# Kernel tuning notes

Measured on AMD Instinct MI355X. Metric: run time of the kernel, lower is better.

## Reference

```python
import jax, jax.numpy as jnp
import numpy as np

N_NODES = 100000
N_EDGES = 400000
IN_FEATS = 64
H_FEATS = 128
INTER = 128
NUM_CLASSES = 64


def setup_inputs() -> dict:
    key = jax.random.key(0)
    ks = jax.random.split(key, 32)
    inp = {}
    inp['gate_type'] = jax.random.randint(ks[0], (N_NODES,), 0, IN_FEATS)
    inp['src'] = jax.random.randint(ks[1], (N_EDGES,), 0, N_NODES)
    inp['dst'] = jax.random.randint(ks[2], (N_EDGES,), 0, N_NODES)
    inp['src_idx'] = jax.random.uniform(ks[3], (N_EDGES,), dtype=jnp.float32)
    inp['dst_idx'] = jax.random.uniform(ks[4], (N_EDGES,), dtype=jnp.float32)
    inp['rev'] = jax.random.uniform(ks[5], (N_EDGES,), dtype=jnp.float32)
    inp['emb'] = jax.random.normal(ks[6], (IN_FEATS, IN_FEATS), dtype=jnp.float32) * 0.05
    dims = [(IN_FEATS, H_FEATS), (H_FEATS, H_FEATS), (H_FEATS, H_FEATS), (H_FEATS, H_FEATS), (H_FEATS, NUM_CLASSES)]
    k = 7
    for i, (fi, fo) in enumerate(dims, 1):
        # xavier-normal-like scaling
        inp[f'w1_{i}'] = jax.random.normal(ks[k], (INTER, fi + 3), dtype=jnp.float32) * np.float32(np.sqrt(2.0 / (fi + 3 + INTER))); k += 1
        inp[f'w2_{i}'] = jax.random.normal(ks[k], (fo, fi + INTER), dtype=jnp.float32) * np.float32(np.sqrt(2.0 / (fi + INTER + fo))); k += 1
        inp[f'b2_{i}'] = jnp.zeros((fo,), dtype=jnp.float32); k += 1
    return inp


def _qconv(h, src, dst, w_edge, W1, W2, b2):
    # message: concat src node feats with edge feats -> [E, d+3]
    m = jnp.concatenate([h[src], w_edge], axis=1)
    # linear1 (no bias) + leaky_relu (torch default slope 0.01)
    tmp = jax.nn.leaky_relu(m @ W1.T, negative_slope=0.01)  # [E, inter]
    # mean-reduce per destination node (isolated nodes -> zeros, matching DGL)
    s = jax.ops.segment_sum(tmp, dst, num_segments=h.shape[0])
    cnt = jax.ops.segment_sum(jnp.ones((dst.shape[0],), tmp.dtype), dst, num_segments=h.shape[0])
    h_N = s / jnp.maximum(cnt, 1.0)[:, None]
    # linear2 on [h, h_N]
    return jnp.concatenate([h, h_N], axis=1) @ W2.T + b2


def reference(gate_type, src, dst, src_idx, dst_idx, rev, emb,
              w1_1, w2_1, b2_1, w1_2, w2_2, b2_2, w1_3, w2_3, b2_3,
              w1_4, w2_4, b2_4, w1_5, w2_5, b2_5):
    h = emb[gate_type]  # [N, in_feats]
    w_edge = jnp.stack([src_idx, dst_idx, rev], axis=1)  # [E, 3]
    layers = [(w1_1, w2_1, b2_1), (w1_2, w2_2, b2_2), (w1_3, w2_3, b2_3),
              (w1_4, w2_4, b2_4), (w1_5, w2_5, b2_5)]
    for i, (W1, W2, b2) in enumerate(layers):
        h = _qconv(h, src, dst, w_edge, W1, W2, b2)
        if i < 4:
            h = jax.nn.relu(h)
    return h
```

## Files before the change

kernel.cpp:

```cpp
#include <hip/hip_runtime.h>
#include <hip/hip_fp16.h>

typedef __attribute__((ext_vector_type(8))) short short8;
typedef __attribute__((ext_vector_type(4))) float f32x4;
typedef unsigned short u16;

__device__ __forceinline__ u16 f2bf(float f) {
    unsigned u = __float_as_uint(f);
    unsigned r = ((u >> 16) & 1) + 0x7FFFu;
    return (u16)((u + r) >> 16);
}

__device__ __forceinline__ void gload_lds16(const void* g, void* l) {
    __builtin_amdgcn_global_load_lds((const __attribute__((address_space(1))) unsigned int*)g,
                                     (__attribute__((address_space(3))) unsigned int*)l,
                                     16, 0, 0);
}

__device__ __forceinline__ unsigned pk_fma(unsigned a, unsigned b, unsigned c) {
    unsigned d;
    asm("v_pk_fma_f16 %0, %1, %2, %3" : "=v"(d) : "v"(a), "v"(b), "v"(c));
    return d;
}
__device__ __forceinline__ unsigned pk_mul(unsigned a, unsigned b) {
    unsigned d;
    asm("v_pk_mul_f16 %0, %1, %2" : "=v"(d) : "v"(a), "v"(b));
    return d;
}
__device__ __forceinline__ unsigned pk_max(unsigned a, unsigned b) {
    unsigned d;
    asm("v_pk_max_f16 %0, %1, %2" : "=v"(d) : "v"(a), "v"(b));
    return d;
}


__global__ void k_count(const int* __restrict__ dst, int* __restrict__ cnt, int E) {
    int i = blockIdx.x * 256 + threadIdx.x;
    if (i < E) atomicAdd(&cnt[dst[i]], 1);
}

__global__ void k_scan1(const int* __restrict__ cnt, int* __restrict__ partial, int N) {
    __shared__ int sm[256];
    int idx = blockIdx.x * 256 + threadIdx.x;
    sm[threadIdx.x] = (idx < N) ? cnt[idx] : 0;
    __syncthreads();
    for (int s = 128; s > 0; s >>= 1) {
        if (threadIdx.x < s) sm[threadIdx.x] += sm[threadIdx.x + s];
        __syncthreads();
    }
    if (threadIdx.x == 0) partial[blockIdx.x] = sm[0];
}

__global__ void k_scan2(int* __restrict__ partial, int nb) {
    __shared__ int sm[512];
    int t = threadIdx.x;
    sm[t] = (t < nb) ? partial[t] : 0;
    __syncthreads();
    for (int off = 1; off < 512; off <<= 1) {
        int v = (t >= off) ? sm[t - off] : 0;
        __syncthreads();
        sm[t] += v;
        __syncthreads();
    }
    if (t < nb) partial[t] = (t == 0) ? 0 : sm[t - 1];
}

__global__ void k_scan3(const int* __restrict__ cnt, const int* __restrict__ partial,
                        int* __restrict__ row_off, int* __restrict__ cursor,
                        float* __restrict__ invdeg, int N, int E) {
    __shared__ int sm[256];
    int idx = blockIdx.x * 256 + threadIdx.x;
    int v = (idx < N) ? cnt[idx] : 0;
    sm[threadIdx.x] = v;
    __syncthreads();
    for (int off = 1; off < 256; off <<= 1) {
        int u = (threadIdx.x >= off) ? sm[threadIdx.x - off] : 0;
        __syncthreads();
        sm[threadIdx.x] += u;
        __syncthreads();
    }
    if (idx < N) {
        int excl = partial[blockIdx.x] + sm[threadIdx.x] - v;
        row_off[idx] = excl;
        cursor[idx] = excl;
        invdeg[idx] = 1.0f / (float)((v > 1) ? v : 1);
    }
    if (idx == 0) row_off[N] = E;
}

__global__ void k_scatter(const int* __restrict__ dst, const int* __restrict__ src,
                          const float* __restrict__ sidx, const float* __restrict__ didx,
                          const float* __restrict__ rev,
                          int* __restrict__ cursor, int4* __restrict__ payload, int E) {
    int i = blockIdx.x * 256 + threadIdx.x;
    if (i < E) {
        int p = atomicAdd(&cursor[dst[i]], 1);
        unsigned hs = (unsigned)__half_as_ushort(__float2half_rn(sidx[i]));
        unsigned hd = (unsigned)__half_as_ushort(__float2half_rn(didx[i]));
        unsigned hr = (unsigned)__half_as_ushort(__float2half_rn(rev[i]));
        int4 v;
        v.x = src[i];
        v.y = (int)(hs * 0x10001u);
        v.z = (int)(hd * 0x10001u);
        v.w = (int)(hr * 0x10001u);
        payload[p] = v;
    }
}


__global__ void k_emb(const int* __restrict__ gt, const float* __restrict__ emb,
                      u16* __restrict__ h0, int N) {
    int i = blockIdx.x * 256 + threadIdx.x;
    if (i < N * 64) {
        int n = i >> 6, f = i & 63;
        h0[i] = f2bf(emb[(gt[n] << 6) | f]);
    }
}


struct WDesc {
    const float* src[10];
    u16* dst[10];
    int scols[10];
    int dcols[10];
    int n[10];
};

__global__ void k_wconv(WDesc d) {
    int seg = blockIdx.y;
    int idx = blockIdx.x * 256 + threadIdx.x;
    if (idx < d.n[seg]) {
        int dc = d.dcols[seg];
        int r = idx / dc, c = idx % dc;
        d.dst[seg][idx] = f2bf(d.src[seg][r * d.scols[seg] + c]);
    }
}

struct EDesc {
    const float* src[5];
    unsigned* dst[5];
    int ldw[5];
    int fi[5];
};

__global__ void k_wedge(EDesc d) {
    int l = blockIdx.x;
    int i = threadIdx.x;
    if (i < 192) {
        int c = i >> 6, j = i & 63;
        float a = d.src[l][(size_t)(2 * j) * d.ldw[l] + d.fi[l] + c];
        float b = d.src[l][(size_t)(2 * j + 1) * d.ldw[l] + d.fi[l] + c];
        unsigned lo = (unsigned)__half_as_ushort(__float2half_rn(a));
        unsigned hi = (unsigned)__half_as_ushort(__float2half_rn(b));
        d.dst[l][(c << 6) + j] = lo | (hi << 16);
    }
}


__global__ __launch_bounds__(256)
void k_edge(int N,
            const int* __restrict__ row_off, const int4* __restrict__ payload,
            const u16* __restrict__ g,
            const unsigned* __restrict__ W1h,
            const float* __restrict__ invdeg,
            u16* __restrict__ hN)
{
    const int t = threadIdx.x;
    const int lane = t & 63;
    const int fl = lane & 15;
    const int eg = lane >> 4;
    const int wid = blockIdx.x * (blockDim.x >> 6) + (t >> 6);
    const int nwtot = gridDim.x * (blockDim.x >> 6);
    const int per = (N + nwtot - 1) / nwtot;
    const int n0 = wid * per;
    if (n0 >= N) return;
    const int n1 = (n0 + per < N) ? (n0 + per) : N;

    const uint4 wa = *(const uint4*)&W1h[(fl << 2)];
    const uint4 wb = *(const uint4*)&W1h[64 + (fl << 2)];
    const uint4 wc = *(const uint4*)&W1h[128 + (fl << 2)];
    const unsigned c001 = ((unsigned)__half_as_ushort(__float2half_rn(0.01f))) * 0x10001u;

    int beg = row_off[n0];
    for (int n = n0; n < n1; ++n) {
        const int end = row_off[n + 1];
        float acc[8] = {0.f, 0.f, 0.f, 0.f, 0.f, 0.f, 0.f, 0.f};

        int p = beg + eg;
        int4 pl;
        if (p < end) pl = payload[p];
        while (p < end) {
            const int pn = p + 4;
            int4 plN = pl;
            if (pn < end) plN = payload[pn];
            const uint4 gv = *(const uint4*)(g + ((size_t)pl.x << 7) + (fl << 3));
            const unsigned si = (unsigned)pl.y;
            const unsigned di = (unsigned)pl.z;
            const unsigned rv = (unsigned)pl.w;
            unsigned v0 = pk_fma(wa.x, si, gv.x);
            unsigned v1 = pk_fma(wa.y, si, gv.y);
            unsigned v2 = pk_fma(wa.z, si, gv.z);
            unsigned v3 = pk_fma(wa.w, si, gv.w);
            v0 = pk_fma(wb.x, di, v0);
            v1 = pk_fma(wb.y, di, v1);
            v2 = pk_fma(wb.z, di, v2);
            v3 = pk_fma(wb.w, di, v3);
            v0 = pk_fma(wc.x, rv, v0);
            v1 = pk_fma(wc.y, rv, v1);
            v2 = pk_fma(wc.z, rv, v2);
            v3 = pk_fma(wc.w, rv, v3);
            v0 = pk_max(v0, pk_mul(v0, c001));
            v1 = pk_max(v1, pk_mul(v1, c001));
            v2 = pk_max(v2, pk_mul(v2, c001));
            v3 = pk_max(v3, pk_mul(v3, c001));
            const float2 f0 = __half22float2(*(const __half2*)&v0);
            const float2 f1 = __half22float2(*(const __half2*)&v1);
            const float2 f2 = __half22float2(*(const __half2*)&v2);
            const float2 f3 = __half22float2(*(const __half2*)&v3);
            acc[0] += f0.x; acc[1] += f0.y;
            acc[2] += f1.x; acc[3] += f1.y;
            acc[4] += f2.x; acc[5] += f2.y;
            acc[6] += f3.x; acc[7] += f3.y;
            p = pn;
            pl = plN;
        }

#pragma unroll
        for (int r = 0; r < 8; r++) {
            acc[r] += __shfl_xor(acc[r], 16, 64);
            acc[r] += __shfl_xor(acc[r], 32, 64);
        }

        if (eg == 0) {
            const float inv = invdeg[n];
            unsigned q0 = (unsigned)f2bf(acc[0] * inv) | ((unsigned)f2bf(acc[1] * inv) << 16);
            unsigned q1 = (unsigned)f2bf(acc[2] * inv) | ((unsigned)f2bf(acc[3] * inv) << 16);
            unsigned q2 = (unsigned)f2bf(acc[4] * inv) | ((unsigned)f2bf(acc[5] * inv) << 16);
            unsigned q3 = (unsigned)f2bf(acc[6] * inv) | ((unsigned)f2bf(acc[7] * inv) << 16);
            uint4 out = make_uint4(q0, q1, q2, q3);
            *(uint4*)(hN + ((size_t)n << 7) + (fl << 3)) = out;
        }
        beg = end;
    }
}


template<int K, int O, int SPLIT, int BIAS, int RELU, int OUTDT>
__global__ __launch_bounds__(256)
void k_mfma(int M,
            const u16* __restrict__ A1, int lda1,
            const u16* __restrict__ A2, int lda2,
            const u16* __restrict__ Wb,
            const float* __restrict__ bias,
            void* __restrict__ Cout, int ldc)
{
    constexpr int KP = K + 8;
    constexpr int NF = O / 32;
    constexpr int WC = O / 2;
    __shared__ __align__(16) u16 Wlds[O * KP];
    __shared__ __align__(16) u16 Atile[128 * 32];

    const int t = threadIdx.x;
    const int m0 = blockIdx.x * 128;
    const int w = t >> 6, l = t & 63;
    const int wm = w & 1, wn = w >> 1;
    const int lr = l & 15, lh = l >> 4;

    for (int idx = t; idx < O * (K / 8); idx += 256) {
        int row = idx / (K / 8), ch = idx % (K / 8);
        uint4 v = *(const uint4*)(Wb + (size_t)row * K + ch * 8);
        *(uint4*)(&Wlds[row * KP + ch * 8]) = v;
    }

    f32x4 acc[4][NF];
#pragma unroll
    for (int mi = 0; mi < 4; mi++)
#pragma unroll
        for (int ni = 0; ni < NF; ni++) acc[mi][ni] = (f32x4){0.f, 0.f, 0.f, 0.f};

    __syncthreads();

    for (int kt = 0; kt < K / 32; ++kt) {
        const int k0 = kt * 32;
        const u16* Asrc;
        int lda, kof;
        if (k0 < SPLIT) { Asrc = A1; lda = lda1; kof = k0; }
        else            { Asrc = A2; lda = lda2; kof = k0 - SPLIT; }
#pragma unroll
        for (int q = 0; q < 2; ++q) {
            int o = q * 4096 + t * 16;
            int row = o >> 6, cb = o & 63;
            int m = m0 + row;
            m = (m < M) ? m : (M - 1);
            gload_lds16(Asrc + (size_t)m * lda + kof + (cb >> 1), (void*)(Atile + (o >> 1)));
        }
        __syncthreads();

        short8 a[4], b[NF];
#pragma unroll
        for (int mi = 0; mi < 4; mi++)
            a[mi] = *(const short8*)(Atile + (wm * 64 + mi * 16 + lr) * 32 + lh * 8);
#pragma unroll
        for (int ni = 0; ni < NF; ni++)
            b[ni] = *(const short8*)(Wlds + (size_t)(wn * WC + ni * 16 + lr) * KP + k0 + lh * 8);
#pragma unroll
        for (int mi = 0; mi < 4; mi++)
#pragma unroll
            for (int ni = 0; ni < NF; ni++)
                acc[mi][ni] = __builtin_amdgcn_mfma_f32_16x16x32_bf16(a[mi], b[ni], acc[mi][ni], 0, 0, 0);
        __syncthreads();
    }

    float bv[NF];
#pragma unroll
    for (int ni = 0; ni < NF; ni++)
        bv[ni] = BIAS ? bias[wn * WC + ni * 16 + lr] : 0.f;
#pragma unroll
    for (int mi = 0; mi < 4; mi++) {
#pragma unroll
        for (int i = 0; i < 4; i++) {
            int row = m0 + wm * 64 + mi * 16 + lh * 4 + i;
            if (row < M) {
#pragma unroll
                for (int ni = 0; ni < NF; ni++) {
                    float v = acc[mi][ni][i] + bv[ni];
                    if (RELU) v = fmaxf(v, 0.f);
                    int col = wn * WC + ni * 16 + lr;
                    if (OUTDT == 1)      ((u16*)Cout)[(size_t)row * ldc + col] = f2bf(v);
                    else if (OUTDT == 2) ((__half*)Cout)[(size_t)row * ldc + col] = __float2half(v);
                    else                 ((float*)Cout)[(size_t)row * ldc + col] = v;
                }
            }
        }
    }
}


extern "C" void kernel_launch(void* const* d_in, const int* in_sizes, int n_in,
                              void* d_out, int out_size, void* d_ws, size_t ws_size,
                              hipStream_t stream)
{
    const int N = in_sizes[0];
    const int E = in_sizes[1];
    const int* gate = (const int*)d_in[0];
    const int* src = (const int*)d_in[1];
    const int* dst = (const int*)d_in[2];
    const float* sidx = (const float*)d_in[3];
    const float* didx = (const float*)d_in[4];
    const float* rev = (const float*)d_in[5];
    const float* emb = (const float*)d_in[6];
    const float* w1[5] = {(const float*)d_in[7], (const float*)d_in[10], (const float*)d_in[13],
                          (const float*)d_in[16], (const float*)d_in[19]};
    const float* w2[5] = {(const float*)d_in[8], (const float*)d_in[11], (const float*)d_in[14],
                          (const float*)d_in[17], (const float*)d_in[20]};
    const float* b2[5] = {(const float*)d_in[9], (const float*)d_in[12], (const float*)d_in[15],
                          (const float*)d_in[18], (const float*)d_in[21]};

    char* ws = (char*)d_ws;
    size_t off = 0;
    auto alloc = [&](size_t bytes) {
        void* p = ws + off;
        off = (off + bytes + 255) & ~(size_t)255;
        return p;
    };
    u16* hb0 = (u16*)alloc((size_t)N * 128 * 2);
    u16* hb1 = (u16*)alloc((size_t)N * 128 * 2);
    u16* hN = (u16*)alloc((size_t)N * 128 * 2);
    u16* g = (u16*)alloc((size_t)N * 128 * 2);
    int* cnt = (int*)alloc((size_t)N * 4);
    int* row_off = (int*)alloc((size_t)(N + 1) * 4);
    int* cursor = (int*)alloc((size_t)N * 4);
    int4* payload = (int4*)alloc((size_t)E * 16);
    int* partial = (int*)alloc(512 * 4);
    float* invd = (float*)alloc((size_t)N * 4);
    unsigned* w1h = (unsigned*)alloc(5 * 192 * 4);
    u16* w1b[5];
    u16* w2b[5];
    const int fis[5] = {64, 128, 128, 128, 128};
    for (int i = 0; i < 5; i++) w1b[i] = (u16*)alloc((size_t)128 * fis[i] * 2);
    for (int i = 0; i < 5; i++) {
        int fo = (i == 4) ? 64 : 128;
        w2b[i] = (u16*)alloc((size_t)fo * (fis[i] + 128) * 2);
    }

    WDesc wd;
    for (int i = 0; i < 5; i++) {
        wd.src[i] = w1[i]; wd.dst[i] = w1b[i];
        wd.scols[i] = fis[i] + 3; wd.dcols[i] = fis[i]; wd.n[i] = 128 * fis[i];
        int fo = (i == 4) ? 64 : 128;
        wd.src[5 + i] = w2[i]; wd.dst[5 + i] = w2b[i];
        wd.scols[5 + i] = fis[i] + 128; wd.dcols[5 + i] = fis[i] + 128;
        wd.n[5 + i] = fo * (fis[i] + 128);
    }
    k_wconv<<<dim3(128, 10), dim3(256), 0, stream>>>(wd);

    EDesc ed;
    for (int i = 0; i < 5; i++) {
        ed.src[i] = w1[i];
        ed.dst[i] = w1h + i * 192;
        ed.ldw[i] = fis[i] + 3;
        ed.fi[i] = fis[i];
    }
    k_wedge<<<dim3(5), dim3(192), 0, stream>>>(ed);

    hipMemsetAsync(cnt, 0, (size_t)N * 4, stream);
    k_count<<<dim3((E + 255) / 256), dim3(256), 0, stream>>>(dst, cnt, E);
    const int nb = (N + 255) / 256;
    k_scan1<<<dim3(nb), dim3(256), 0, stream>>>(cnt, partial, N);
    k_scan2<<<dim3(1), dim3(512), 0, stream>>>(partial, nb);
    k_scan3<<<dim3(nb), dim3(256), 0, stream>>>(cnt, partial, row_off, cursor, invd, N, E);
    k_scatter<<<dim3((E + 255) / 256), dim3(256), 0, stream>>>(dst, src, sidx, didx, rev, cursor, payload, E);
    k_emb<<<dim3((N * 64 + 255) / 256), dim3(256), 0, stream>>>(gate, emb, hb0, N);

    u16* hcur = hb0;
    u16* hnxt = hb1;
    const int gg = (N + 127) / 128;
    const int eb = 2048;

    k_mfma<64, 128, 64, 0, 0, 2><<<dim3(gg), dim3(256), 0, stream>>>(
        N, hcur, 64, (const u16*)nullptr, 0, w1b[0], (const float*)nullptr, g, 128);
    k_edge<<<dim3(eb), dim3(256), 0, stream>>>(N, row_off, payload, g, w1h + 0 * 192, invd, hN);
    k_mfma<192, 128, 64, 1, 1, 1><<<dim3(gg), dim3(256), 0, stream>>>(
        N, hcur, 64, hN, 128, w2b[0], b2[0], hnxt, 128);
    hcur = hb1; hnxt = hb0;

    for (int l = 1; l < 4; ++l) {
        k_mfma<128, 128, 128, 0, 0, 2><<<dim3(gg), dim3(256), 0, stream>>>(
            N, hcur, 128, (const u16*)nullptr, 0, w1b[l], (const float*)nullptr, g, 128);
        k_edge<<<dim3(eb), dim3(256), 0, stream>>>(N, row_off, payload, g, w1h + l * 192, invd, hN);
        k_mfma<256, 128, 128, 1, 1, 1><<<dim3(gg), dim3(256), 0, stream>>>(
            N, hcur, 128, hN, 128, w2b[l], b2[l], hnxt, 128);
        u16* tmp = hcur; hcur = hnxt; hnxt = tmp;
    }

    k_mfma<128, 128, 128, 0, 0, 2><<<dim3(gg), dim3(256), 0, stream>>>(
        N, hcur, 128, (const u16*)nullptr, 0, w1b[4], (const float*)nullptr, g, 128);
    k_edge<<<dim3(eb), dim3(256), 0, stream>>>(N, row_off, payload, g, w1h + 4 * 192, invd, hN);
    k_mfma<256, 64, 128, 1, 0, 0><<<dim3(gg), dim3(256), 0, stream>>>(
        N, hcur, 128, hN, 128, w2b[4], b2[4], (float*)d_out, 64);
}
```

Measured before the change: 454.8 us.

## Fuse layer output GEMM with next layer's node projection GEMM

Adds a fused kernel that computes the linear2 output for a 128-row tile, applies bias and ReLU, writes h, and keeps the tile in LDS. It then multiplies that tile by the next layer's W1 node weights to produce the fp16 per-node projection used by the edge kernel. This removes four separate projection GEMM launches and the re-read of h from global memory. In exchange the kernel uses more LDS, aliasing the W tile with the H tile, which may lower occupancy and serialises two GEMMs within each block.

```diff
diff --git a/kernel.cpp b/kernel.cpp
--- a/kernel.cpp
+++ b/kernel.cpp
@@ -336,6 +336,143 @@
 }
 
 
+template<int K, int SPLIT>
+__global__ __launch_bounds__(256)
+void k_mfma_fused(int M,
+                  const u16* __restrict__ A1, int lda1,
+                  const u16* __restrict__ A2, int lda2,
+                  const u16* __restrict__ Wb,
+                  const float* __restrict__ bias,
+                  u16* __restrict__ Hout,
+                  const u16* __restrict__ Wg,
+                  u16* __restrict__ Gout)
+{
+    constexpr int KP = K + 8;
+    constexpr int HP = 136;
+    __shared__ __align__(16) char U[(128 * HP * 2) * 2 + 128 * 32 * 2];
+    u16* Wlds  = (u16*)U;
+    u16* Htile = (u16*)U;
+    u16* Wglds = (u16*)(U + 128 * HP * 2);
+    u16* Atile = (u16*)(U + 2 * 128 * HP * 2);
+
+    const int t = threadIdx.x;
+    const int m0 = blockIdx.x * 128;
+    const int w = t >> 6, l = t & 63;
+    const int wm = w & 1, wn = w >> 1;
+    const int lr = l & 15, lh = l >> 4;
+
+    for (int idx = t; idx < 128 * (K / 8); idx += 256) {
+        int row = idx / (K / 8), ch = idx % (K / 8);
+        uint4 v = *(const uint4*)(Wb + (size_t)row * K + ch * 8);
+        *(uint4*)(&Wlds[row * KP + ch * 8]) = v;
+    }
+
+    f32x4 acc[4][4];
+#pragma unroll
+    for (int mi = 0; mi < 4; mi++)
+#pragma unroll
+        for (int ni = 0; ni < 4; ni++) acc[mi][ni] = (f32x4){0.f, 0.f, 0.f, 0.f};
+
+    __syncthreads();
+
+    for (int kt = 0; kt < K / 32; ++kt) {
+        const int k0 = kt * 32;
+        const u16* Asrc;
+        int lda, kof;
+        if (k0 < SPLIT) { Asrc = A1; lda = lda1; kof = k0; }
+        else            { Asrc = A2; lda = lda2; kof = k0 - SPLIT; }
+#pragma unroll
+        for (int q = 0; q < 2; ++q) {
+            int o = q * 4096 + t * 16;
+            int row = o >> 6, cb = o & 63;
+            int m = m0 + row;
+            m = (m < M) ? m : (M - 1);
+            gload_lds16(Asrc + (size_t)m * lda + kof + (cb >> 1), (void*)(Atile + (o >> 1)));
+        }
+        __syncthreads();
+
+        short8 a[4], b[4];
+#pragma unroll
+        for (int mi = 0; mi < 4; mi++)
+            a[mi] = *(const short8*)(Atile + (wm * 64 + mi * 16 + lr) * 32 + lh * 8);
+#pragma unroll
+        for (int ni = 0; ni < 4; ni++)
+            b[ni] = *(const short8*)(Wlds + (size_t)(wn * 64 + ni * 16 + lr) * KP + k0 + lh * 8);
+#pragma unroll
+        for (int mi = 0; mi < 4; mi++)
+#pragma unroll
+            for (int ni = 0; ni < 4; ni++)
+                acc[mi][ni] = __builtin_amdgcn_mfma_f32_16x16x32_bf16(a[mi], b[ni], acc[mi][ni], 0, 0, 0);
+        __syncthreads();
+    }
+
+    for (int idx = t; idx < 128 * 16; idx += 256) {
+        int row = idx >> 4, ch = idx & 15;
+        uint4 v = *(const uint4*)(Wg + (size_t)row * 128 + ch * 8);
+        *(uint4*)(&Wglds[row * HP + ch * 8]) = v;
+    }
+
+    float bv[4];
+#pragma unroll
+    for (int ni = 0; ni < 4; ni++) bv[ni] = bias[wn * 64 + ni * 16 + lr];
+#pragma unroll
+    for (int mi = 0; mi < 4; mi++) {
+#pragma unroll
+        for (int i = 0; i < 4; i++) {
+            int rloc = wm * 64 + mi * 16 + lh * 4 + i;
+            int row = m0 + rloc;
+#pragma unroll
+            for (int ni = 0; ni < 4; ni++) {
+                float v = fmaxf(acc[mi][ni][i] + bv[ni], 0.f);
+                u16 hv = f2bf(v);
+                int col = wn * 64 + ni * 16 + lr;
+                Htile[rloc * HP + col] = hv;
+                if (row < M) Hout[(size_t)row * 128 + col] = hv;
+            }
+        }
+    }
+    __syncthreads();
+
+    f32x4 acc2[4][4];
+#pragma unroll
+    for (int mi = 0; mi < 4; mi++)
+#pragma unroll
+        for (int ni = 0; ni < 4; ni++) acc2[mi][ni] = (f32x4){0.f, 0.f, 0.f, 0.f};
+
+#pragma unroll
+    for (int kt = 0; kt < 4; ++kt) {
+        const int k0 = kt * 32;
+        short8 a[4], b[4];
+#pragma unroll
+        for (int mi = 0; mi < 4; mi++)
+            a[mi] = *(const short8*)(Htile + (wm * 64 + mi * 16 + lr) * HP + k0 + lh * 8);
+#pragma unroll
+        for (int ni = 0; ni < 4; ni++)
+            b[ni] = *(const short8*)(Wglds + (wn * 64 + ni * 16 + lr) * HP + k0 + lh * 8);
+#pragma unroll
+        for (int mi = 0; mi < 4; mi++)
+#pragma unroll
+            for (int ni = 0; ni < 4; ni++)
+                acc2[mi][ni] = __builtin_amdgcn_mfma_f32_16x16x32_bf16(a[mi], b[ni], acc2[mi][ni], 0, 0, 0);
+    }
+
+#pragma unroll
+    for (int mi = 0; mi < 4; mi++) {
+#pragma unroll
+        for (int i = 0; i < 4; i++) {
+            int row = m0 + wm * 64 + mi * 16 + lh * 4 + i;
+            if (row < M) {
+#pragma unroll
+                for (int ni = 0; ni < 4; ni++) {
+                    int col = wn * 64 + ni * 16 + lr;
+                    ((__half*)Gout)[(size_t)row * 128 + col] = __float2half(acc2[mi][ni][i]);
+                }
+            }
+        }
+    }
+}
+
+
 extern "C" void kernel_launch(void* const* d_in, const int* in_sizes, int n_in,
                               void* d_out, int out_size, void* d_ws, size_t ws_size,
                               hipStream_t stream)
@@ -412,29 +549,24 @@
     k_scatter<<<dim3((E + 255) / 256), dim3(256), 0, stream>>>(dst, src, sidx, didx, rev, cursor, payload, E);
     k_emb<<<dim3((N * 64 + 255) / 256), dim3(256), 0, stream>>>(gate, emb, hb0, N);
 
-    u16* hcur = hb0;
-    u16* hnxt = hb1;
     const int gg = (N + 127) / 128;
     const int eb = 2048;
 
     k_mfma<64, 128, 64, 0, 0, 2><<<dim3(gg), dim3(256), 0, stream>>>(
-        N, hcur, 64, (const u16*)nullptr, 0, w1b[0], (const float*)nullptr, g, 128);
+        N, hb0, 64, (const u16*)nullptr, 0, w1b[0], (const float*)nullptr, g, 128);
     k_edge<<<dim3(eb), dim3(256), 0, stream>>>(N, row_off, payload, g, w1h + 0 * 192, invd, hN);
-    k_mfma<192, 128, 64, 1, 1, 1><<<dim3(gg), dim3(256), 0, stream>>>(
-        N, hcur, 64, hN, 128, w2b[0], b2[0], hnxt, 128);
-    hcur = hb1; hnxt = hb0;
-
+    k_mfma_fused<192, 64><<<dim3(gg), dim3(256), 0, stream>>>(
+        N, hb0, 64, hN, 128, w2b[0], b2[0], hb1, w1b[1], g);
+
+    u16* hcur = hb1;
+    u16* hnxt = hb0;
     for (int l = 1; l < 4; ++l) {
-        k_mfma<128, 128, 128, 0, 0, 2><<<dim3(gg), dim3(256), 0, stream>>>(
-            N, hcur, 128, (const u16*)nullptr, 0, w1b[l], (const float*)nullptr, g, 128);
         k_edge<<<dim3(eb), dim3(256), 0, stream>>>(N, row_off, payload, g, w1h + l * 192, invd, hN);
-        k_mfma<256, 128, 128, 1, 1, 1><<<dim3(gg), dim3(256), 0, stream>>>(
-            N, hcur, 128, hN, 128, w2b[l], b2[l], hnxt, 128);
+        k_mfma_fused<256, 128><<<dim3(gg), dim3(256), 0, stream>>>(
+            N, hcur, 128, hN, 128, w2b[l], b2[l], hnxt, w1b[l + 1], g);
         u16* tmp = hcur; hcur = hnxt; hnxt = tmp;
     }
 
-    k_mfma<128, 128, 128, 0, 0, 2><<<dim3(gg), dim3(256), 0, stream>>>(
-        N, hcur, 128, (const u16*)nullptr, 0, w1b[4], (const float*)nullptr, g, 128);
     k_edge<<<dim3(eb), dim3(256), 0, stream>>>(N, row_off, payload, g, w1h + 4 * 192, invd, hN);
     k_mfma<256, 64, 128, 1, 0, 0><<<dim3(gg), dim3(256), 0, stream>>>(
         N, hcur, 128, hN, 128, w2b[4], b2[4], (float*)d_out, 64);
```

Measured after the change: 426.4 us. 1.07x faster.

## Fuse next layer's W1 projection into linear2 GEMM epilogue; drop LDS staging

Applied to the files above, without the earlier changes.

The linear2 GEMM now stages its bf16 output tile in swizzled LDS and immediately multiplies it by the next layer's W1 node-part, writing the fp16 projection g directly. This removes four separate projection GEMM launches and their re-read of h from global memory. The GEMM's A and W operands are now loaded straight from global memory into registers instead of being staged through LDS with barriers, and launch bounds request 4 blocks per CU. This relies on cache for operand reuse and raises register and LDS pressure in the fused variant.

```diff
diff --git a/kernel.cpp b/kernel.cpp
--- a/kernel.cpp
+++ b/kernel.cpp
@@ -9,12 +9,6 @@
     unsigned u = __float_as_uint(f);
     unsigned r = ((u >> 16) & 1) + 0x7FFFu;
     return (u16)((u + r) >> 16);
-}
-
-__device__ __forceinline__ void gload_lds16(const void* g, void* l) {
-    __builtin_amdgcn_global_load_lds((const __attribute__((address_space(1))) unsigned int*)g,
-                                     (__attribute__((address_space(3))) unsigned int*)l,
-                                     16, 0, 0);
 }
 
 __device__ __forceinline__ unsigned pk_fma(unsigned a, unsigned b, unsigned c) {
@@ -245,20 +239,20 @@
 }
 
 
-template<int K, int O, int SPLIT, int BIAS, int RELU, int OUTDT>
-__global__ __launch_bounds__(256)
-void k_mfma(int M,
+template<int K, int O, int SPLIT, int BIAS, int RELU, int OUTDT, int FUSE>
+__global__ __launch_bounds__(256, 4)
+void k_gemm(int M,
             const u16* __restrict__ A1, int lda1,
             const u16* __restrict__ A2, int lda2,
-            const u16* __restrict__ Wb,
+            const u16* __restrict__ W,
             const float* __restrict__ bias,
-            void* __restrict__ Cout, int ldc)
+            void* __restrict__ Cout, int ldc,
+            const u16* __restrict__ Wg,
+            u16* __restrict__ Gout)
 {
-    constexpr int KP = K + 8;
     constexpr int NF = O / 32;
     constexpr int WC = O / 2;
-    __shared__ __align__(16) u16 Wlds[O * KP];
-    __shared__ __align__(16) u16 Atile[128 * 32];
+    __shared__ __align__(16) char Hbuf[FUSE ? 128 * 256 : 16];
 
     const int t = threadIdx.x;
     const int m0 = blockIdx.x * 128;
@@ -266,10 +260,11 @@
     const int wm = w & 1, wn = w >> 1;
     const int lr = l & 15, lh = l >> 4;
 
-    for (int idx = t; idx < O * (K / 8); idx += 256) {
-        int row = idx / (K / 8), ch = idx % (K / 8);
-        uint4 v = *(const uint4*)(Wb + (size_t)row * K + ch * 8);
-        *(uint4*)(&Wlds[row * KP + ch * 8]) = v;
+    int arow[4];
+#pragma unroll
+    for (int mi = 0; mi < 4; mi++) {
+        int m = m0 + wm * 64 + mi * 16 + lr;
+        arow[mi] = (m < M) ? m : (M - 1);
     }
 
     f32x4 acc[4][NF];
@@ -278,37 +273,25 @@
 #pragma unroll
         for (int ni = 0; ni < NF; ni++) acc[mi][ni] = (f32x4){0.f, 0.f, 0.f, 0.f};
 
-    __syncthreads();
-
+#pragma unroll
     for (int kt = 0; kt < K / 32; ++kt) {
         const int k0 = kt * 32;
-        const u16* Asrc;
+        const u16* Abase;
         int lda, kof;
-        if (k0 < SPLIT) { Asrc = A1; lda = lda1; kof = k0; }
-        else            { Asrc = A2; lda = lda2; kof = k0 - SPLIT; }
-#pragma unroll
-        for (int q = 0; q < 2; ++q) {
-            int o = q * 4096 + t * 16;
-            int row = o >> 6, cb = o & 63;
-            int m = m0 + row;
-            m = (m < M) ? m : (M - 1);
-            gload_lds16(Asrc + (size_t)m * lda + kof + (cb >> 1), (void*)(Atile + (o >> 1)));
-        }
-        __syncthreads();
-
+        if (k0 < SPLIT) { Abase = A1; lda = lda1; kof = k0; }
+        else            { Abase = A2; lda = lda2; kof = k0 - SPLIT; }
         short8 a[4], b[NF];
 #pragma unroll
         for (int mi = 0; mi < 4; mi++)
-            a[mi] = *(const short8*)(Atile + (wm * 64 + mi * 16 + lr) * 32 + lh * 8);
+            a[mi] = *(const short8*)(Abase + (size_t)arow[mi] * lda + kof + lh * 8);
 #pragma unroll
         for (int ni = 0; ni < NF; ni++)
-            b[ni] = *(const short8*)(Wlds + (size_t)(wn * WC + ni * 16 + lr) * KP + k0 + lh * 8);
+            b[ni] = *(const short8*)(W + (size_t)(wn * WC + ni * 16 + lr) * K + k0 + lh * 8);
 #pragma unroll
         for (int mi = 0; mi < 4; mi++)
 #pragma unroll
             for (int ni = 0; ni < NF; ni++)
                 acc[mi][ni] = __builtin_amdgcn_mfma_f32_16x16x32_bf16(a[mi], b[ni], acc[mi][ni], 0, 0, 0);
-        __syncthreads();
     }
 
     float bv[NF];
@@ -319,16 +302,64 @@
     for (int mi = 0; mi < 4; mi++) {
 #pragma unroll
         for (int i = 0; i < 4; i++) {
-            int row = m0 + wm * 64 + mi * 16 + lh * 4 + i;
-            if (row < M) {
-#pragma unroll
-                for (int ni = 0; ni < NF; ni++) {
-                    float v = acc[mi][ni][i] + bv[ni];
-                    if (RELU) v = fmaxf(v, 0.f);
-                    int col = wn * WC + ni * 16 + lr;
+            int rloc = wm * 64 + mi * 16 + lh * 4 + i;
+            int row = m0 + rloc;
+#pragma unroll
+            for (int ni = 0; ni < NF; ni++) {
+                float v = acc[mi][ni][i] + bv[ni];
+                if (RELU) v = fmaxf(v, 0.f);
+                int col = wn * WC + ni * 16 + lr;
+                if (FUSE) {
+                    u16 hv = f2bf(v);
+                    *(u16*)(Hbuf + rloc * 256 + ((col * 2) ^ ((rloc & 15) << 4))) = hv;
+                    if (row < M) ((u16*)Cout)[(size_t)row * ldc + col] = hv;
+                } else if (row < M) {
                     if (OUTDT == 1)      ((u16*)Cout)[(size_t)row * ldc + col] = f2bf(v);
                     else if (OUTDT == 2) ((__half*)Cout)[(size_t)row * ldc + col] = __float2half(v);
                     else                 ((float*)Cout)[(size_t)row * ldc + col] = v;
+                }
+            }
+        }
+    }
+
+    if (FUSE) {
+        __syncthreads();
+        f32x4 acc2[4][4];
+#pragma unroll
+        for (int mi = 0; mi < 4; mi++)
+#pragma unroll
+            for (int ni = 0; ni < 4; ni++) acc2[mi][ni] = (f32x4){0.f, 0.f, 0.f, 0.f};
+
+#pragma unroll
+        for (int kt = 0; kt < 4; ++kt) {
+            const int k0 = kt * 32;
+            short8 a[4], b[4];
+#pragma unroll
+            for (int mi = 0; mi < 4; mi++) {
+                int r = wm * 64 + mi * 16 + lr;
+                a[mi] = *(const short8*)(Hbuf + r * 256 + (((k0 + lh * 8) * 2) ^ ((r & 15) << 4)));
+            }
+#pragma unroll
+            for (int ni = 0; ni < 4; ni++)
+                b[ni] = *(const short8*)(Wg + (size_t)(wn * 64 + ni * 16 + lr) * 128 + k0 + lh * 8);
+#pragma unroll
+            for (int mi = 0; mi < 4; mi++)
+#pragma unroll
+                for (int ni = 0; ni < 4; ni++)
+                    acc2[mi][ni] = __builtin_amdgcn_mfma_f32_16x16x32_bf16(a[mi], b[ni], acc2[mi][ni], 0, 0, 0);
+        }
+
+#pragma unroll
+        for (int mi = 0; mi < 4; mi++) {
+#pragma unroll
+            for (int i = 0; i < 4; i++) {
+                int row = m0 + wm * 64 + mi * 16 + lh * 4 + i;
+                if (row < M) {
+#pragma unroll
+                    for (int ni = 0; ni < 4; ni++) {
+                        int col = wn * 64 + ni * 16 + lr;
+                        ((__half*)Gout)[(size_t)row * 128 + col] = __float2half(acc2[mi][ni][i]);
+                    }
                 }
             }
         }
@@ -412,30 +443,27 @@
     k_scatter<<<dim3((E + 255) / 256), dim3(256), 0, stream>>>(dst, src, sidx, didx, rev, cursor, payload, E);
     k_emb<<<dim3((N * 64 + 255) / 256), dim3(256), 0, stream>>>(gate, emb, hb0, N);
 
-    u16* hcur = hb0;
-    u16* hnxt = hb1;
     const int gg = (N + 127) / 128;
     const int eb = 2048;
 
-    k_mfma<64, 128, 64, 0, 0, 2><<<dim3(gg), dim3(256), 0, stream>>>(
-        N, hcur, 64, (const u16*)nullptr, 0, w1b[0], (const float*)nullptr, g, 128);
+    k_gemm<64, 128, 64, 0, 0, 2, 0><<<dim3(gg), dim3(256), 0, stream>>>(
+        N, hb0, 64, (const u16*)nullptr, 0, w1b[0], (const float*)nullptr, g, 128,
+        (const u16*)nullptr, (u16*)nullptr);
     k_edge<<<dim3(eb), dim3(256), 0, stream>>>(N, row_off, payload, g, w1h + 0 * 192, invd, hN);
-    k_mfma<192, 128, 64, 1, 1, 1><<<dim3(gg), dim3(256), 0, stream>>>(
-        N, hcur, 64, hN, 128, w2b[0], b2[0], hnxt, 128);
-    hcur = hb1; hnxt = hb0;
-
+    k_gemm<192, 128, 64, 1, 1, 1, 1><<<dim3(gg), dim3(256), 0, stream>>>(
+        N, hb0, 64, hN, 128, w2b[0], b2[0], hb1, 128, w1b[1], g);
+
+    u16* hcur = hb1;
+    u16* hnxt = hb0;
     for (int l = 1; l < 4; ++l) {
-        k_mfma<128, 128, 128, 0, 0, 2><<<dim3(gg), dim3(256), 0, stream>>>(
-            N, hcur, 128, (const u16*)nullptr, 0, w1b[l], (const float*)nullptr, g, 128);
         k_edge<<<dim3(eb), dim3(256), 0, stream>>>(N, row_off, payload, g, w1h + l * 192, invd, hN);
-        k_mfma<256, 128, 128, 1, 1, 1><<<dim3(gg), dim3(256), 0, stream>>>(
-            N, hcur, 128, hN, 128, w2b[l], b2[l], hnxt, 128);
+        k_gemm<256, 128, 128, 1, 1, 1, 1><<<dim3(gg), dim3(256), 0, stream>>>(
+            N, hcur, 128, hN, 128, w2b[l], b2[l], hnxt, 128, w1b[l + 1], g);
         u16* tmp = hcur; hcur = hnxt; hnxt = tmp;
     }
 
-    k_mfma<128, 128, 128, 0, 0, 2><<<dim3(gg), dim3(256), 0, stream>>>(
-        N, hcur, 128, (const u16*)nullptr, 0, w1b[4], (const float*)nullptr, g, 128);
     k_edge<<<dim3(eb), dim3(256), 0, stream>>>(N, row_off, payload, g, w1h + 4 * 192, invd, hN);
-    k_mfma<256, 64, 128, 1, 0, 0><<<dim3(gg), dim3(256), 0, stream>>>(
-        N, hcur, 128, hN, 128, w2b[4], b2[4], (float*)d_out, 64);
-}
+    k_gemm<256, 64, 128, 1, 0, 0, 0><<<dim3(gg), dim3(256), 0, stream>>>(
+        N, hcur, 128, hN, 128, w2b[4], b2[4], (float*)d_out, 64,
+        (const u16*)nullptr, (u16*)nullptr);
+}
```

Result: slower. 476.7 us (+4.8%).
